# Kernel optimization log

Hardware: AMD Instinct MI355X
Metric: run time of the kernel (lower is better)

Reference implementation:

```python
import jax, jax.numpy as jnp
import numpy as np
import math

B, M, DM = 8, 512, 1024
H, DH = 16, 64
DFF = 4096
RA, RF, RO = 32, 384, 384
EPS = 1e-12  # BERT LayerNorm eps


def layernorm(x, g, b):
    mu = jnp.mean(x, axis=-1, keepdims=True)
    var = jnp.mean(jnp.square(x - mu), axis=-1, keepdims=True)
    return (x - mu) * jax.lax.rsqrt(var + EPS) * g + b


def setup_inputs() -> dict:
    key = jax.random.key(0)
    ks = jax.random.split(key, 24)
    s = 0.02
    inp = {
        "x": jax.random.normal(ks[0], (B, M, DM), jnp.float32),
        "mask": jnp.zeros((B, M), jnp.float32),  # additive attention mask
        "Pq": jax.random.normal(ks[1], (H, DM, RA), jnp.float32) * s,
        "Vq": jax.random.normal(ks[2], (H, RA, DH), jnp.float32) * s,
        "Pk": jax.random.normal(ks[3], (H, DM, RA), jnp.float32) * s,
        "Vk": jax.random.normal(ks[4], (H, RA, DH), jnp.float32) * s,
        "Pv": jax.random.normal(ks[5], (H, DM, RA), jnp.float32) * s,
        "Vv": jax.random.normal(ks[6], (H, RA, DH), jnp.float32) * s,
        "bq": jax.random.normal(ks[7], (H, DH), jnp.float32) * s,
        "bk": jax.random.normal(ks[8], (H, DH), jnp.float32) * s,
        "bv": jax.random.normal(ks[9], (H, DH), jnp.float32) * s,
        "Uo": jax.random.normal(ks[10], (DM, RO), jnp.float32) * s,
        "Vo": jax.random.normal(ks[11], (RO, DM), jnp.float32) * s,
        "bo_attn": jax.random.normal(ks[12], (DM,), jnp.float32) * s,
        "U1": jax.random.normal(ks[13], (DM, RF), jnp.float32) * s,
        "V1": jax.random.normal(ks[14], (RF, DFF), jnp.float32) * s,
        "b1": jax.random.normal(ks[15], (DFF,), jnp.float32) * s,
        "U2": jax.random.normal(ks[16], (DFF, RF), jnp.float32) * s,
        "V2": jax.random.normal(ks[17], (RF, DM), jnp.float32) * s,
        "b2": jax.random.normal(ks[18], (DM,), jnp.float32) * s,
        "ln1_g": jnp.ones((DM,), jnp.float32),
        "ln1_b": jnp.zeros((DM,), jnp.float32),
        "ln2_g": jnp.ones((DM,), jnp.float32),
        "ln2_b": jnp.zeros((DM,), jnp.float32),
    }
    return inp


def reference(x, mask, Pq, Vq, Pk, Vk, Pv, Vv, bq, bk, bv,
              Uo, Vo, bo_attn, U1, V1, b1, U2, V2, b2,
              ln1_g, ln1_b, ln2_g, ln2_b):
    b_, m_, dm = x.shape
    h = Pq.shape[0]
    dh = dm // h
    # low-rank per-head projections: x -> [B,H,M,R] -> [B,H,M,dh]
    q = jnp.einsum('bmd,hdr->bhmr', x, Pq)
    k = jnp.einsum('bmd,hdr->bhmr', x, Pk)
    v = jnp.einsum('bmd,hdr->bhmr', x, Pv)
    Q = jnp.einsum('bhmr,hrd->bhmd', q, Vq) + bq[None, :, None, :]
    K = jnp.einsum('bhmr,hrd->bhmd', k, Vk) + bk[None, :, None, :]
    V = jnp.einsum('bhmr,hrd->bhmd', v, Vv) + bv[None, :, None, :]
    # scaled dot-product attention (flash_svd_attention equivalent)
    scores = jnp.einsum('bhmd,bhnd->bhmn', Q, K) / math.sqrt(dh)
    scores = scores + mask[:, None, None, :]
    probs = jax.nn.softmax(scores, axis=-1)
    attn = jnp.einsum('bhmn,bhnd->bhmd', probs, V)  # [B,H,M,dh]
    attn = attn.transpose(0, 2, 1, 3).reshape(b_, m_, dm)
    # low-rank output projection + residual + LN
    x1 = layernorm(x + (attn @ Uo) @ Vo + bo_attn, ln1_g, ln1_b)
    # flashsvd_ffn_v1 equivalent: gelu((x1 @ U1) @ V1 + b1) @ U2 @ V2 + b2
    mid = x1 @ U1
    hdn = jax.nn.gelu(mid @ V1 + b1, approximate=False)
    y = (hdn @ U2) @ V2 + b2
    out = layernorm(x1 + y, ln2_g, ln2_b)
    return out
```

## Files before the change

### kernel.cpp

```cpp
#include <hip/hip_runtime.h>
#include <math.h>

typedef __attribute__((ext_vector_type(8))) short short8;
typedef __attribute__((ext_vector_type(4))) float floatx4;

__device__ inline unsigned short f2bf(float f){
    union { float f; unsigned u; } v; v.f = f;
    unsigned r = v.u + 0x7fffu + ((v.u >> 16) & 1u);
    return (unsigned short)(r >> 16);
}
__device__ inline float bf2f(unsigned short b){
    union { unsigned u; float f; } v; v.u = ((unsigned)b) << 16;
    return v.f;
}
__device__ inline unsigned short to_bf(float f){ return f2bf(f); }
__device__ inline unsigned short to_bf(unsigned short u){ return u; }

#define GLD_LDS16(g, l) __builtin_amdgcn_global_load_lds( \
    (const __attribute__((address_space(1))) void*)(g),   \
    (__attribute__((address_space(3))) void*)(l), 16, 0, 0)

__global__ __launch_bounds__(256) void cast_kernel(const float* __restrict__ s,
                                                   unsigned short* __restrict__ d){
    int i = (blockIdx.x*256 + threadIdx.x)*4;
    float4 v = *(const float4*)(s+i);
    ushort4 o; o.x=f2bf(v.x); o.y=f2bf(v.y); o.z=f2bf(v.z); o.w=f2bf(v.w);
    *(ushort4*)(d+i) = o;
}

__global__ __launch_bounds__(256) void castP_kernel(
    const float* __restrict__ p0, const float* __restrict__ p1,
    const float* __restrict__ p2, unsigned short* __restrict__ d){
    int blk = blockIdx.x;
    int proj = blk >> 9;
    const float* s = (proj==0)?p0:(proj==1)?p1:p2;
    int off = (blk & 511)*1024 + threadIdx.x*4;
    float4 v = *(const float4*)(s+off);
    ushort4 o; o.x=f2bf(v.x); o.y=f2bf(v.y); o.z=f2bf(v.z); o.w=f2bf(v.w);
    *(ushort4*)(d + (size_t)proj*524288 + off) = o;
}

__global__ __launch_bounds__(256) void reduce4_kernel(
    const float* __restrict__ p, unsigned short* __restrict__ o, long mn){
    long i = ((long)blockIdx.x*256 + threadIdx.x)*4;
    float4 a = *(const float4*)(p+i);
    float4 b = *(const float4*)(p+mn+i);
    float4 c = *(const float4*)(p+2*mn+i);
    float4 d = *(const float4*)(p+3*mn+i);
    ushort4 r;
    r.x = f2bf(a.x+b.x+c.x+d.x); r.y = f2bf(a.y+b.y+c.y+d.y);
    r.z = f2bf(a.z+b.z+c.z+d.z); r.w = f2bf(a.w+b.w+c.w+d.w);
    *(ushort4*)(o+i) = r;
}

__global__ __launch_bounds__(256) void bcat_kernel(
    const float* __restrict__ bq, const float* __restrict__ bk,
    const float* __restrict__ bv, float* __restrict__ bcat){
    int i = blockIdx.x*256 + threadIdx.x;
    const float* p = (i < 1024) ? bq : (i < 2048) ? bk : bv;
    bcat[i] = p[i & 1023];
}

template<typename T>
__global__ __launch_bounds__(256) void trans_kernel(
    const T* __restrict__ src, unsigned short* __restrict__ dst,
    int R, int C, long sz, long dz)
{
    __shared__ unsigned short tile[32][33];
    const T* s = src + (size_t)blockIdx.z * sz;
    unsigned short* d = dst + (size_t)blockIdx.z * dz;
    int c0 = blockIdx.x*32, r0 = blockIdx.y*32;
    int tr = threadIdx.x>>3, tc = (threadIdx.x&7)*4;
    const T* sp = s + (size_t)(r0+tr)*C + c0 + tc;
#pragma unroll
    for (int i=0;i<4;i++) tile[tr][tc+i] = to_bf(sp[i]);
    __syncthreads();
    ushort4 o; o.x = tile[tc+0][tr]; o.y = tile[tc+1][tr];
    o.z = tile[tc+2][tr]; o.w = tile[tc+3][tr];
    *(ushort4*)(d + (size_t)(c0+tr)*R + r0 + tc) = o;
}

__global__ __launch_bounds__(256) void trans2_kernel(
    const float* __restrict__ s0, unsigned short* __restrict__ d0,
    const float* __restrict__ s1, unsigned short* __restrict__ d1,
    int R, int C)
{
    __shared__ unsigned short tile[32][33];
    const float* s = blockIdx.z ? s1 : s0;
    unsigned short* d = blockIdx.z ? d1 : d0;
    int c0 = blockIdx.x*32, r0 = blockIdx.y*32;
    int tr = threadIdx.x>>3, tc = (threadIdx.x&7)*4;
    const float* sp = s + (size_t)(r0+tr)*C + c0 + tc;
#pragma unroll
    for (int i=0;i<4;i++) tile[tr][tc+i] = f2bf(sp[i]);
    __syncthreads();
    ushort4 o; o.x = tile[tc+0][tr]; o.y = tile[tc+1][tr];
    o.z = tile[tc+2][tr]; o.w = tile[tc+3][tr];
    *(ushort4*)(d + (size_t)(c0+tr)*R + r0 + tc) = o;
}

__global__ __launch_bounds__(256) void vtrans3_kernel(
    const float* __restrict__ v0, const float* __restrict__ v1,
    const float* __restrict__ v2, unsigned short* __restrict__ dst)
{
    __shared__ unsigned short tile[32][33];
    int z = blockIdx.z;
    int proj = z >> 4, h = z & 15;
    const float* s = ((proj==0)?v0:(proj==1)?v1:v2) + h*2048;
    unsigned short* d = dst + (size_t)proj*32768 + h*2048;
    int c0 = blockIdx.x*32;
    int tr = threadIdx.x>>3, tc = (threadIdx.x&7)*4;
    const float* sp = s + (size_t)tr*64 + c0 + tc;
#pragma unroll
    for (int i=0;i<4;i++) tile[tr][tc+i] = f2bf(sp[i]);
    __syncthreads();
    ushort4 o; o.x = tile[tc+0][tr]; o.y = tile[tc+1][tr];
    o.z = tile[tc+2][tr]; o.w = tile[tc+3][tr];
    *(ushort4*)(d + (size_t)(c0+tr)*32 + tc) = o;
}

__global__ __launch_bounds__(256) void mm64_kernel(
    const unsigned short* __restrict__ A, const unsigned short* __restrict__ Bt,
    unsigned short* __restrict__ C, int Kdim, int lda, int ldb, int ldc,
    long ah, long al, long bh, long bl, long ch, long cl)
{
    __shared__ unsigned short As[64*40];
    __shared__ unsigned short Bs[64*40];
    int z = blockIdx.z;
    const unsigned short* Ab = A + (size_t)(z>>4)*ah + (size_t)(z&15)*al;
    const unsigned short* Bb = Bt + (size_t)(z>>4)*bh + (size_t)(z&15)*bl;
    int row0 = blockIdx.y*64, col0 = blockIdx.x*64;
    int t = threadIdx.x;
    int ar = t>>2, ak = (t&3)*8;
    int w = t>>6, lane = t&63, quad = lane>>4, c16 = lane&15;
    int wm = (w&1)*32, wn = (w>>1)*32;

    floatx4 zero = {0.f,0.f,0.f,0.f};
    floatx4 acc[2][2];
    acc[0][0]=zero; acc[0][1]=zero; acc[1][0]=zero; acc[1][1]=zero;

    const unsigned short* Ap = Ab + (size_t)(row0+ar)*lda + ak;
    const unsigned short* Bp = Bb + (size_t)(col0+ar)*ldb + ak;

    for (int kk=0; kk<Kdim; kk+=32){
        uint4 av = *(const uint4*)(Ap + kk);
        uint4 bv = *(const uint4*)(Bp + kk);
        __syncthreads();
        *(uint4*)(As + ar*40 + ak) = av;
        *(uint4*)(Bs + ar*40 + ak) = bv;
        __syncthreads();
        short8 a0 = *(const short8*)(As + (wm   +c16)*40 + quad*8);
        short8 a1 = *(const short8*)(As + (wm+16+c16)*40 + quad*8);
        short8 b0 = *(const short8*)(Bs + (wn   +c16)*40 + quad*8);
        short8 b1 = *(const short8*)(Bs + (wn+16+c16)*40 + quad*8);
        acc[0][0] = __builtin_amdgcn_mfma_f32_16x16x32_bf16(a0,b0,acc[0][0],0,0,0);
        acc[0][1] = __builtin_amdgcn_mfma_f32_16x16x32_bf16(a0,b1,acc[0][1],0,0,0);
        acc[1][0] = __builtin_amdgcn_mfma_f32_16x16x32_bf16(a1,b0,acc[1][0],0,0,0);
        acc[1][1] = __builtin_amdgcn_mfma_f32_16x16x32_bf16(a1,b1,acc[1][1],0,0,0);
    }

    size_t zc = (size_t)(z>>4)*ch + (size_t)(z&15)*cl;
#pragma unroll
    for (int mt=0; mt<2; mt++)
#pragma unroll
    for (int r=0; r<4; r++){
        int row = row0 + wm + mt*16 + quad*4 + r;
#pragma unroll
        for (int nt=0; nt<2; nt++){
            int col = col0 + wn + nt*16 + c16;
            C[zc + (size_t)row*ldc + col] = f2bf(acc[mt][nt][r]);
        }
    }
}

template<int EPI>
__global__ __launch_bounds__(256) void mm128_kernel(
    const unsigned short* __restrict__ A, const unsigned short* __restrict__ Bt,
    void* __restrict__ C, int Kdim, int lda, int ldb, int ldc,
    const float* __restrict__ aux, const float* __restrict__ resid)
{
    __shared__ unsigned short As[128*64];
    __shared__ unsigned short Bs[128*64];
    int row0 = blockIdx.y*128, col0 = blockIdx.x*128;
    int t = threadIdx.x;
    int w = t>>6, lane = t&63, quad = lane>>4, c16 = lane&15;
    int wm = (w&1)*64, wn = (w>>1)*64;

    int srow = lane>>3;
    int kc = (lane&7) ^ srow;
    const unsigned short* Ag = A + (size_t)(row0 + w*32 + srow)*lda + kc*8;
    const unsigned short* Bg = Bt + (size_t)(col0 + w*32 + srow)*ldb + kc*8;
    unsigned short* AsW = As + (w*32)*64;
    unsigned short* BsW = Bs + (w*32)*64;

    floatx4 acc[4][4];
#pragma unroll
    for (int i=0;i<4;i++)
#pragma unroll
    for (int j=0;j<4;j++) acc[i][j] = (floatx4){0.f,0.f,0.f,0.f};

    int xa = (c16&7)*8;

    for (int kk=0; kk<Kdim; kk+=64){
#pragma unroll
        for (int i=0;i<4;i++){
            GLD_LDS16(Ag + (size_t)(i*8)*lda + kk, AsW + i*512);
            GLD_LDS16(Bg + (size_t)(i*8)*ldb + kk, BsW + i*512);
        }
        __syncthreads();
#pragma unroll
        for (int ks=0; ks<2; ks++){
            short8 a[4], b[4];
#pragma unroll
            for (int mt=0; mt<4; mt++)
                a[mt] = *(const short8*)(As + (wm + mt*16 + c16)*64
                                            + (((ks*4 + quad)*8) ^ xa));
#pragma unroll
            for (int nt=0; nt<4; nt++)
                b[nt] = *(const short8*)(Bs + (wn + nt*16 + c16)*64
                                            + (((ks*4 + quad)*8) ^ xa));
#pragma unroll
            for (int mt=0; mt<4; mt++)
#pragma unroll
                for (int nt=0; nt<4; nt++)
                    acc[mt][nt] = __builtin_amdgcn_mfma_f32_16x16x32_bf16(
                        a[mt], b[nt], acc[mt][nt], 0,0,0);
        }
        __syncthreads();
    }

#pragma unroll
    for (int mt=0; mt<4; mt++)
#pragma unroll
    for (int r=0; r<4; r++){
        int row = row0 + wm + mt*16 + quad*4 + r;
#pragma unroll
        for (int nt=0; nt<4; nt++){
            int col = col0 + wn + nt*16 + c16;
            float v = acc[mt][nt][r];
            if (EPI==0) {
                ((unsigned short*)C)[(size_t)row*ldc + col] = f2bf(v);
            } else if (EPI==2) {
                v += aux[col];
                v = 0.5f*v*(1.0f + erff(v*0.70710678118654752f));
                ((unsigned short*)C)[(size_t)row*ldc + col] = f2bf(v);
            } else if (EPI==3) {
                ((float*)C)[(size_t)row*ldc + col] =
                    v + aux[col] + resid[(size_t)row*ldc + col];
            } else {
                int proj = col >> 10, cw = col & 1023;
                int b_ = row >> 9, m_ = row & 511;
                size_t idx = (size_t)proj*4194304
                           + ((size_t)(b_*16 + (cw>>6))*512 + m_)*64 + (cw&63);
                ((unsigned short*)C)[idx] = f2bf(v + aux[col]);
            }
        }
    }
}

__global__ __launch_bounds__(256) void mmsk_kernel(
    const unsigned short* __restrict__ A, const unsigned short* __restrict__ Bt,
    float* __restrict__ Cp, int Kchunk, int lda, int ldb, int ldc, long mn)
{
    __shared__ unsigned short As[128*64];
    __shared__ unsigned short Bs[128*64];
    int row0 = blockIdx.y*128, col0 = blockIdx.x*128;
    int t = threadIdx.x;
    int w = t>>6, lane = t&63, quad = lane>>4, c16 = lane&15;
    int wm = (w&1)*64, wn = (w>>1)*64;

    int srow = lane>>3;
    int kc = (lane&7) ^ srow;
    const unsigned short* Ag = A + (size_t)(row0 + w*32 + srow)*lda + kc*8;
    const unsigned short* Bg = Bt + (size_t)(col0 + w*32 + srow)*ldb + kc*8;
    unsigned short* AsW = As + (w*32)*64;
    unsigned short* BsW = Bs + (w*32)*64;

    floatx4 acc[4][4];
#pragma unroll
    for (int i=0;i<4;i++)
#pragma unroll
    for (int j=0;j<4;j++) acc[i][j] = (floatx4){0.f,0.f,0.f,0.f};

    int xa = (c16&7)*8;
    int k0 = blockIdx.z * Kchunk;
    for (int kk=k0; kk<k0+Kchunk; kk+=64){
#pragma unroll
        for (int i=0;i<4;i++){
            GLD_LDS16(Ag + (size_t)(i*8)*lda + kk, AsW + i*512);
            GLD_LDS16(Bg + (size_t)(i*8)*ldb + kk, BsW + i*512);
        }
        __syncthreads();
#pragma unroll
        for (int ks=0; ks<2; ks++){
            short8 a[4], b[4];
#pragma unroll
            for (int mt=0; mt<4; mt++)
                a[mt] = *(const short8*)(As + (wm + mt*16 + c16)*64
                                            + (((ks*4 + quad)*8) ^ xa));
#pragma unroll
            for (int nt=0; nt<4; nt++)
                b[nt] = *(const short8*)(Bs + (wn + nt*16 + c16)*64
                                            + (((ks*4 + quad)*8) ^ xa));
#pragma unroll
            for (int mt=0; mt<4; mt++)
#pragma unroll
                for (int nt=0; nt<4; nt++)
                    acc[mt][nt] = __builtin_amdgcn_mfma_f32_16x16x32_bf16(
                        a[mt], b[nt], acc[mt][nt], 0,0,0);
        }
        __syncthreads();
    }

    float* Cz = Cp + (size_t)blockIdx.z * mn;
#pragma unroll
    for (int mt=0; mt<4; mt++)
#pragma unroll
    for (int r=0; r<4; r++){
        int row = row0 + wm + mt*16 + quad*4 + r;
#pragma unroll
        for (int nt=0; nt<4; nt++){
            int col = col0 + wn + nt*16 + c16;
            Cz[(size_t)row*ldc + col] = acc[mt][nt][r];
        }
    }
}

__global__ __launch_bounds__(256) void flash_kernel(
    const unsigned short* __restrict__ Qb, const unsigned short* __restrict__ Kb,
    const unsigned short* __restrict__ Vt, const float* __restrict__ mask,
    unsigned short* __restrict__ attn)
{
    __shared__ unsigned short Qs[128*64];
    __shared__ unsigned short Ks[64*64];
    __shared__ unsigned short Vts[64*64];
    __shared__ unsigned short Ps[4][32*68];

    int qt = blockIdx.x, bh = blockIdx.y;
    int b = bh >> 4, h = bh & 15;
    int t = threadIdx.x;
    int w = t>>6, lane = t&63, quad = lane>>4, c16 = lane&15;

    const unsigned short* Qtile = Qb + ((size_t)bh*512 + qt*128)*64;
    const unsigned short* Ktile0 = Kb + (size_t)bh*512*64;
    const unsigned short* Vtbh = Vt + (size_t)bh*32768;

#pragma unroll
    for (int i=0;i<4;i++){
        GLD_LDS16(Qtile + (size_t)(w*32 + i*8)*64 + lane*8, Qs + (w*32+i*8)*64);
    }

    floatx4 Oacc[2][4];
#pragma unroll
    for (int mt=0;mt<2;mt++)
#pragma unroll
    for (int nd=0;nd<4;nd++) Oacc[mt][nd] = (floatx4){0.f,0.f,0.f,0.f};
    float mrow[2][4], lrow[2][4];
#pragma unroll
    for (int mt=0;mt<2;mt++)
#pragma unroll
    for (int r=0;r<4;r++){ mrow[mt][r] = -3.0e38f; lrow[mt][r] = 0.f; }

    unsigned short* Pw = &Ps[w][0];

    for (int kt=0; kt<8; kt++){
        __syncthreads();
#pragma unroll
        for (int i=0;i<2;i++){
            GLD_LDS16(Ktile0 + (size_t)(kt*64 + w*16 + i*8)*64 + lane*8,
                      Ks + (w*16+i*8)*64);
            GLD_LDS16(Vtbh + (size_t)(w*16 + i*8 + (lane>>3))*512 + kt*64 + (lane&7)*8,
                      Vts + (w*16+i*8)*64);
        }
        __syncthreads();

        floatx4 Sacc[2][4];
#pragma unroll
        for (int mt=0;mt<2;mt++)
#pragma unroll
        for (int nt=0;nt<4;nt++) Sacc[mt][nt] = (floatx4){0.f,0.f,0.f,0.f};
#pragma unroll
        for (int ks=0; ks<2; ks++){
            short8 a[2], bfr[4];
#pragma unroll
            for (int mt=0;mt<2;mt++)
                a[mt] = *(const short8*)(Qs + (w*32 + mt*16 + c16)*64 + ks*32 + quad*8);
#pragma unroll
            for (int nt=0;nt<4;nt++)
                bfr[nt] = *(const short8*)(Ks + (nt*16 + c16)*64 + ks*32 + quad*8);
#pragma unroll
            for (int mt=0;mt<2;mt++)
#pragma unroll
            for (int nt=0;nt<4;nt++)
                Sacc[mt][nt] = __builtin_amdgcn_mfma_f32_16x16x32_bf16(
                    a[mt], bfr[nt], Sacc[mt][nt], 0,0,0);
        }

        float mv[4];
#pragma unroll
        for (int nt=0;nt<4;nt++)
            mv[nt] = mask[b*512 + kt*64 + nt*16 + c16];

#pragma unroll
        for (int mt=0;mt<2;mt++)
#pragma unroll
        for (int r=0;r<4;r++){
            float sv[4];
#pragma unroll
            for (int nt=0;nt<4;nt++) sv[nt] = Sacc[mt][nt][r]*0.125f + mv[nt];
            float rmax = fmaxf(fmaxf(sv[0],sv[1]), fmaxf(sv[2],sv[3]));
            rmax = fmaxf(rmax, __shfl_xor(rmax, 1));
            rmax = fmaxf(rmax, __shfl_xor(rmax, 2));
            rmax = fmaxf(rmax, __shfl_xor(rmax, 4));
            rmax = fmaxf(rmax, __shfl_xor(rmax, 8));
            float mold = mrow[mt][r];
            float mnew = fmaxf(mold, rmax);
            float alpha = __expf(mold - mnew);
            float p[4], ps = 0.f;
#pragma unroll
            for (int nt=0;nt<4;nt++){ p[nt] = __expf(sv[nt]-mnew); ps += p[nt]; }
            ps += __shfl_xor(ps, 1);
            ps += __shfl_xor(ps, 2);
            ps += __shfl_xor(ps, 4);
            ps += __shfl_xor(ps, 8);
            lrow[mt][r] = lrow[mt][r]*alpha + ps;
            mrow[mt][r] = mnew;
#pragma unroll
            for (int nd=0;nd<4;nd++) Oacc[mt][nd][r] *= alpha;
#pragma unroll
            for (int nt=0;nt<4;nt++)
                Pw[(mt*16 + quad*4 + r)*68 + nt*16 + c16] = f2bf(p[nt]);
        }

#pragma unroll
        for (int ks=0; ks<2; ks++){
            short8 a[2], bfr[4];
#pragma unroll
            for (int mt=0;mt<2;mt++)
                a[mt] = *(const short8*)(Pw + (mt*16 + c16)*68 + ks*32 + quad*8);
#pragma unroll
            for (int nd=0;nd<4;nd++)
                bfr[nd] = *(const short8*)(Vts + (nd*16 + c16)*64 + ks*32 + quad*8);
#pragma unroll
            for (int mt=0;mt<2;mt++)
#pragma unroll
            for (int nd=0;nd<4;nd++)
                Oacc[mt][nd] = __builtin_amdgcn_mfma_f32_16x16x32_bf16(
                    a[mt], bfr[nd], Oacc[mt][nd], 0,0,0);
        }
    }

#pragma unroll
    for (int mt=0;mt<2;mt++)
#pragma unroll
    for (int r=0;r<4;r++){
        int m = qt*128 + w*32 + mt*16 + quad*4 + r;
        float inv = 1.0f / lrow[mt][r];
        unsigned short* op = attn + ((size_t)(b*512 + m))*1024 + h*64;
#pragma unroll
        for (int nd=0;nd<4;nd++)
            op[nd*16 + c16] = f2bf(Oacc[mt][nd][r] * inv);
    }
}

template<int DUAL>
__global__ __launch_bounds__(256) void ln_kernel(
    const float* __restrict__ in, const float* __restrict__ g,
    const float* __restrict__ bta, float* __restrict__ outf,
    unsigned short* __restrict__ outb)
{
    int row = blockIdx.x;
    int t = threadIdx.x;
    const float* x = in + (size_t)row*1024;
    float4 xv = ((const float4*)x)[t];
    float s  = xv.x + xv.y + xv.z + xv.w;
    float ss = xv.x*xv.x + xv.y*xv.y + xv.z*xv.z + xv.w*xv.w;
#pragma unroll
    for (int off=32; off>0; off>>=1){ s += __shfl_down(s, off); ss += __shfl_down(ss, off); }
    __shared__ float rs[4], rss[4];
    int wid = t>>6, lane = t&63;
    if (lane==0){ rs[wid]=s; rss[wid]=ss; }
    __syncthreads();
    s  = rs[0]+rs[1]+rs[2]+rs[3];
    ss = rss[0]+rss[1]+rss[2]+rss[3];
    float mu  = s * (1.0f/1024.0f);
    float var = ss * (1.0f/1024.0f) - mu*mu;
    float inv = rsqrtf(var + 1e-12f);
    float4 gv = ((const float4*)g)[t];
    float4 bv = ((const float4*)bta)[t];
    float4 o = make_float4((xv.x-mu)*inv*gv.x+bv.x, (xv.y-mu)*inv*gv.y+bv.y,
                           (xv.z-mu)*inv*gv.z+bv.z, (xv.w-mu)*inv*gv.w+bv.w);
    ((float4*)(outf + (size_t)row*1024))[t] = o;
    if (DUAL){
        ushort4 ob; ob.x=f2bf(o.x); ob.y=f2bf(o.y); ob.z=f2bf(o.z); ob.w=f2bf(o.w);
        ((ushort4*)(outb + (size_t)row*1024))[t] = ob;
    }
}

extern "C" void kernel_launch(void* const* d_in, const int* in_sizes, int n_in,
                              void* d_out, int out_size, void* d_ws, size_t ws_size,
                              hipStream_t stream)
{
    const float* x       = (const float*)d_in[0];
    const float* mask    = (const float*)d_in[1];
    const float* Pq      = (const float*)d_in[2];
    const float* Vq      = (const float*)d_in[3];
    const float* Pk      = (const float*)d_in[4];
    const float* Vk      = (const float*)d_in[5];
    const float* Pv      = (const float*)d_in[6];
    const float* Vv      = (const float*)d_in[7];
    const float* bq      = (const float*)d_in[8];
    const float* bk      = (const float*)d_in[9];
    const float* bv      = (const float*)d_in[10];
    const float* Uo      = (const float*)d_in[11];
    const float* Vo      = (const float*)d_in[12];
    const float* bo_attn = (const float*)d_in[13];
    const float* U1      = (const float*)d_in[14];
    const float* V1      = (const float*)d_in[15];
    const float* b1      = (const float*)d_in[16];
    const float* U2      = (const float*)d_in[17];
    const float* V2      = (const float*)d_in[18];
    const float* b2      = (const float*)d_in[19];
    const float* ln1_g   = (const float*)d_in[20];
    const float* ln1_b   = (const float*)d_in[21];
    const float* ln2_g   = (const float*)d_in[22];
    const float* ln2_b   = (const float*)d_in[23];
    float* out = (float*)d_out;

    char* base = (char*)d_ws;
    unsigned short* Uo_t   = (unsigned short*)(base + 0);
    unsigned short* Vo_t   = (unsigned short*)(base + 786432);
    unsigned short* U1_t   = (unsigned short*)(base + 1572864);
    unsigned short* V1_t   = (unsigned short*)(base + 2359296);
    unsigned short* U2_t   = (unsigned short*)(base + 5505024);
    unsigned short* V2_t   = (unsigned short*)(base + 8650752);
    float*          bcat   = (float*)(base + 9437184);
    unsigned short* Wt     = (unsigned short*)(base + 9449472);
    unsigned short* Pbf    = (unsigned short*)(base + 15740928);
    unsigned short* Vt2    = (unsigned short*)(base + 18886656);
    unsigned short* x_bf   = (unsigned short*)(base + 19083264);
    unsigned short* t_bf   = (unsigned short*)(base + 9449472);
    float*          ybuf   = (float*)(base + 12595200);
    float*          x1     = (float*)(base + 29372416);
    unsigned short* x1_bf  = (unsigned short*)(base + 46149632);
    unsigned short* hdn_bf = (unsigned short*)(base + 54538240);
    float*          part0  = (float*)(base + 12595200);
    float*          part1  = (float*)(base + 54538240);
    float*          part2  = (float*)(base + 88092672);
    unsigned short* Qb     = (unsigned short*)(base + 76558336);
    unsigned short* Kb     = (unsigned short*)(base + 84946944);
    unsigned short* Vb     = (unsigned short*)(base + 93535552);
    unsigned short* Vt     = (unsigned short*)(base + 101924160);
    unsigned short* attn_bf= (unsigned short*)(base + 110312768);

    const long MN384 = 4096L*384;

    cast_kernel<<<4096,256,0,stream>>>(x, x_bf);
    castP_kernel<<<1536,256,0,stream>>>(Pq, Pk, Pv, Pbf);
    vtrans3_kernel<<<dim3(2,1,48),256,0,stream>>>(Vq, Vk, Vv, Vt2);
    bcat_kernel<<<12,256,0,stream>>>(bq, bk, bv, bcat);
    trans2_kernel<<<dim3(12,32,2),256,0,stream>>>(Uo, Uo_t, U1, U1_t, 1024, 384);
    trans2_kernel<<<dim3(32,12,2),256,0,stream>>>(Vo, Vo_t, V2, V2_t, 384, 1024);
    trans_kernel<float><<<dim3(128,12,1),256,0,stream>>>(V1, V1_t, 384,4096, 0,0);
    trans_kernel<float><<<dim3(12,128,1),256,0,stream>>>(U2, U2_t, 4096,384, 0,0);

    mm64_kernel<<<dim3(16,1,48),256,0,stream>>>(Vt2, Pbf, Wt,
        32, 32, 32, 1024, 32768,2048, 524288,32768, 1048576,65536);

    mm128_kernel<4><<<dim3(24,32,1),256,0,stream>>>(x_bf, Wt, Qb,
        1024, 1024, 1024, 3072, bcat, nullptr);

    trans_kernel<unsigned short><<<dim3(2,16,128),256,0,stream>>>(Vb, Vt, 512,64, 32768,32768);

    flash_kernel<<<dim3(4,128),256,0,stream>>>(Qb, Kb, Vt, mask, attn_bf);

    mmsk_kernel<<<dim3(3,32,4),256,0,stream>>>(attn_bf, Uo_t, part0,
        256, 1024, 1024, 384, MN384);
    reduce4_kernel<<<1536,256,0,stream>>>(part0, t_bf, MN384);
    mm128_kernel<3><<<dim3(8,32,1),256,0,stream>>>(t_bf, Vo_t, ybuf,
        384, 384, 384, 1024, bo_attn, x);
    ln_kernel<1><<<4096,256,0,stream>>>(ybuf, ln1_g, ln1_b, x1, x1_bf);
    mmsk_kernel<<<dim3(3,32,4),256,0,stream>>>(x1_bf, U1_t, part1,
        256, 1024, 1024, 384, MN384);
    reduce4_kernel<<<1536,256,0,stream>>>(part1, t_bf, MN384);
    mm128_kernel<2><<<dim3(32,32,1),256,0,stream>>>(t_bf, V1_t, hdn_bf,
        384, 384, 384, 4096, b1, nullptr);
    mmsk_kernel<<<dim3(3,32,4),256,0,stream>>>(hdn_bf, U2_t, part2,
        1024, 4096, 4096, 384, MN384);
    reduce4_kernel<<<1536,256,0,stream>>>(part2, t_bf, MN384);
    mm128_kernel<3><<<dim3(8,32,1),256,0,stream>>>(t_bf, V2_t, ybuf,
        384, 384, 384, 1024, b2, x1);
    ln_kernel<0><<<4096,256,0,stream>>>(ybuf, ln2_g, ln2_b, out, nullptr);
}
```

Measured before the change: 378.6 us.

## Fuse V transpose and Q scaling into QKV epilogue; restructure flash attention tiles

The QKV GEMM epilogue now writes V directly in transposed layout and pre-scales Q by 1/sqrt(dh), which removes the separate V transpose kernel and the per-score scale multiply. The flash kernel now processes 64 query rows per block with 16 rows per wave, so the grid doubles. Q fragments are held in registers instead of LDS, the mask is folded into the accumulator init, and K/V/P LDS tiles use an XOR swizzle to avoid bank conflicts. The epilogue's V stores become strided scatter writes, and K/V tiles are reloaded twice as often across blocks.

Result: no change. 375.2 us (-0.9%).

```diff
diff --git a/kernel.cpp b/kernel.cpp
--- a/kernel.cpp
+++ b/kernel.cpp
@@ -250,9 +250,15 @@
             } else {
                 int proj = col >> 10, cw = col & 1023;
                 int b_ = row >> 9, m_ = row & 511;
-                size_t idx = (size_t)proj*4194304
-                           + ((size_t)(b_*16 + (cw>>6))*512 + m_)*64 + (cw&63);
-                ((unsigned short*)C)[idx] = f2bf(v + aux[col]);
+                int hh = cw >> 6, dd = cw & 63;
+                float vv = v + aux[col];
+                if (proj == 0) vv *= 0.125f;
+                size_t idx;
+                if (proj == 2)
+                    idx = (size_t)2*4194304 + ((size_t)(b_*16+hh)*64 + dd)*512 + m_;
+                else
+                    idx = (size_t)proj*4194304 + ((size_t)(b_*16+hh)*512 + m_)*64 + dd;
+                ((unsigned short*)C)[idx] = f2bf(vv);
             }
         }
     }
@@ -331,35 +337,33 @@
     const unsigned short* __restrict__ Vt, const float* __restrict__ mask,
     unsigned short* __restrict__ attn)
 {
-    __shared__ unsigned short Qs[128*64];
     __shared__ unsigned short Ks[64*64];
     __shared__ unsigned short Vts[64*64];
-    __shared__ unsigned short Ps[4][32*68];
+    __shared__ unsigned short Ps[4][16*64];
 
     int qt = blockIdx.x, bh = blockIdx.y;
     int b = bh >> 4, h = bh & 15;
     int t = threadIdx.x;
     int w = t>>6, lane = t&63, quad = lane>>4, c16 = lane&15;
 
-    const unsigned short* Qtile = Qb + ((size_t)bh*512 + qt*128)*64;
+    int qrow = qt*64 + w*16 + c16;
+    const unsigned short* Qp = Qb + ((size_t)bh*512 + qrow)*64 + quad*8;
+    short8 qf0 = *(const short8*)(Qp);
+    short8 qf1 = *(const short8*)(Qp + 32);
+
     const unsigned short* Ktile0 = Kb + (size_t)bh*512*64;
     const unsigned short* Vtbh = Vt + (size_t)bh*32768;
 
-#pragma unroll
-    for (int i=0;i<4;i++){
-        GLD_LDS16(Qtile + (size_t)(w*32 + i*8)*64 + lane*8, Qs + (w*32+i*8)*64);
-    }
-
-    floatx4 Oacc[2][4];
-#pragma unroll
-    for (int mt=0;mt<2;mt++)
-#pragma unroll
-    for (int nd=0;nd<4;nd++) Oacc[mt][nd] = (floatx4){0.f,0.f,0.f,0.f};
-    float mrow[2][4], lrow[2][4];
-#pragma unroll
-    for (int mt=0;mt<2;mt++)
-#pragma unroll
-    for (int r=0;r<4;r++){ mrow[mt][r] = -3.0e38f; lrow[mt][r] = 0.f; }
+    int srow = lane>>3;
+    int kc = (lane&7) ^ srow;
+    int xa = (c16&7)*8;
+
+    floatx4 Oacc[4];
+#pragma unroll
+    for (int nd=0;nd<4;nd++) Oacc[nd] = (floatx4){0.f,0.f,0.f,0.f};
+    float mrow[4], lrow[4];
+#pragma unroll
+    for (int r=0;r<4;r++){ mrow[r] = -3.0e38f; lrow[r] = 0.f; }
 
     unsigned short* Pw = &Ps[w][0];
 
@@ -367,99 +371,88 @@
         __syncthreads();
 #pragma unroll
         for (int i=0;i<2;i++){
-            GLD_LDS16(Ktile0 + (size_t)(kt*64 + w*16 + i*8)*64 + lane*8,
+            GLD_LDS16(Ktile0 + (size_t)(kt*64 + w*16 + i*8 + srow)*64 + kc*8,
                       Ks + (w*16+i*8)*64);
-            GLD_LDS16(Vtbh + (size_t)(w*16 + i*8 + (lane>>3))*512 + kt*64 + (lane&7)*8,
+            GLD_LDS16(Vtbh + (size_t)(w*16 + i*8 + srow)*512 + kt*64 + kc*8,
                       Vts + (w*16+i*8)*64);
         }
         __syncthreads();
 
-        floatx4 Sacc[2][4];
-#pragma unroll
-        for (int mt=0;mt<2;mt++)
-#pragma unroll
-        for (int nt=0;nt<4;nt++) Sacc[mt][nt] = (floatx4){0.f,0.f,0.f,0.f};
+        floatx4 Sacc[4];
+#pragma unroll
+        for (int nt=0;nt<4;nt++){
+            float mv = mask[b*512 + kt*64 + nt*16 + c16];
+            Sacc[nt] = (floatx4){mv,mv,mv,mv};
+        }
 #pragma unroll
         for (int ks=0; ks<2; ks++){
-            short8 a[2], bfr[4];
-#pragma unroll
-            for (int mt=0;mt<2;mt++)
-                a[mt] = *(const short8*)(Qs + (w*32 + mt*16 + c16)*64 + ks*32 + quad*8);
+            short8 qk = ks ? qf1 : qf0;
+            short8 bfr[4];
 #pragma unroll
             for (int nt=0;nt<4;nt++)
-                bfr[nt] = *(const short8*)(Ks + (nt*16 + c16)*64 + ks*32 + quad*8);
-#pragma unroll
-            for (int mt=0;mt<2;mt++)
+                bfr[nt] = *(const short8*)(Ks + (nt*16 + c16)*64
+                                              + (((ks*4 + quad)*8) ^ xa));
 #pragma unroll
             for (int nt=0;nt<4;nt++)
-                Sacc[mt][nt] = __builtin_amdgcn_mfma_f32_16x16x32_bf16(
-                    a[mt], bfr[nt], Sacc[mt][nt], 0,0,0);
-        }
-
-        float mv[4];
-#pragma unroll
-        for (int nt=0;nt<4;nt++)
-            mv[nt] = mask[b*512 + kt*64 + nt*16 + c16];
-
-#pragma unroll
-        for (int mt=0;mt<2;mt++)
+                Sacc[nt] = __builtin_amdgcn_mfma_f32_16x16x32_bf16(
+                    qk, bfr[nt], Sacc[nt], 0,0,0);
+        }
+
 #pragma unroll
         for (int r=0;r<4;r++){
-            float sv[4];
-#pragma unroll
-            for (int nt=0;nt<4;nt++) sv[nt] = Sacc[mt][nt][r]*0.125f + mv[nt];
-            float rmax = fmaxf(fmaxf(sv[0],sv[1]), fmaxf(sv[2],sv[3]));
+            float sv0 = Sacc[0][r], sv1 = Sacc[1][r],
+                  sv2 = Sacc[2][r], sv3 = Sacc[3][r];
+            float rmax = fmaxf(fmaxf(sv0,sv1), fmaxf(sv2,sv3));
             rmax = fmaxf(rmax, __shfl_xor(rmax, 1));
             rmax = fmaxf(rmax, __shfl_xor(rmax, 2));
             rmax = fmaxf(rmax, __shfl_xor(rmax, 4));
             rmax = fmaxf(rmax, __shfl_xor(rmax, 8));
-            float mold = mrow[mt][r];
+            float mold = mrow[r];
             float mnew = fmaxf(mold, rmax);
             float alpha = __expf(mold - mnew);
-            float p[4], ps = 0.f;
-#pragma unroll
-            for (int nt=0;nt<4;nt++){ p[nt] = __expf(sv[nt]-mnew); ps += p[nt]; }
+            float p0 = __expf(sv0-mnew), p1 = __expf(sv1-mnew);
+            float p2 = __expf(sv2-mnew), p3 = __expf(sv3-mnew);
+            float ps = p0+p1+p2+p3;
             ps += __shfl_xor(ps, 1);
             ps += __shfl_xor(ps, 2);
             ps += __shfl_xor(ps, 4);
             ps += __shfl_xor(ps, 8);
-            lrow[mt][r] = lrow[mt][r]*alpha + ps;
-            mrow[mt][r] = mnew;
-#pragma unroll
-            for (int nd=0;nd<4;nd++) Oacc[mt][nd][r] *= alpha;
-#pragma unroll
-            for (int nt=0;nt<4;nt++)
-                Pw[(mt*16 + quad*4 + r)*68 + nt*16 + c16] = f2bf(p[nt]);
+            lrow[r] = lrow[r]*alpha + ps;
+            mrow[r] = mnew;
+#pragma unroll
+            for (int nd=0;nd<4;nd++) Oacc[nd][r] *= alpha;
+            int rl = quad*4 + r;
+            int rx = rl & 7;
+            int cb = rl*64 + (c16&7);
+            Pw[cb + (((0*2 + (c16>>3)) ^ rx)*8)] = f2bf(p0);
+            Pw[cb + (((1*2 + (c16>>3)) ^ rx)*8)] = f2bf(p1);
+            Pw[cb + (((2*2 + (c16>>3)) ^ rx)*8)] = f2bf(p2);
+            Pw[cb + (((3*2 + (c16>>3)) ^ rx)*8)] = f2bf(p3);
         }
 
 #pragma unroll
         for (int ks=0; ks<2; ks++){
-            short8 a[2], bfr[4];
-#pragma unroll
-            for (int mt=0;mt<2;mt++)
-                a[mt] = *(const short8*)(Pw + (mt*16 + c16)*68 + ks*32 + quad*8);
+            short8 pa = *(const short8*)(Pw + c16*64 + (((ks*4 + quad)*8) ^ xa));
+            short8 bfr[4];
 #pragma unroll
             for (int nd=0;nd<4;nd++)
-                bfr[nd] = *(const short8*)(Vts + (nd*16 + c16)*64 + ks*32 + quad*8);
-#pragma unroll
-            for (int mt=0;mt<2;mt++)
+                bfr[nd] = *(const short8*)(Vts + (nd*16 + c16)*64
+                                               + (((ks*4 + quad)*8) ^ xa));
 #pragma unroll
             for (int nd=0;nd<4;nd++)
-                Oacc[mt][nd] = __builtin_amdgcn_mfma_f32_16x16x32_bf16(
-                    a[mt], bfr[nd], Oacc[mt][nd], 0,0,0);
-        }
-    }
-
-#pragma unroll
-    for (int mt=0;mt<2;mt++)
+                Oacc[nd] = __builtin_amdgcn_mfma_f32_16x16x32_bf16(
+                    pa, bfr[nd], Oacc[nd], 0,0,0);
+        }
+    }
+
 #pragma unroll
     for (int r=0;r<4;r++){
-        int m = qt*128 + w*32 + mt*16 + quad*4 + r;
-        float inv = 1.0f / lrow[mt][r];
+        int m = qt*64 + w*16 + quad*4 + r;
+        float inv = 1.0f / lrow[r];
         unsigned short* op = attn + ((size_t)(b*512 + m))*1024 + h*64;
 #pragma unroll
         for (int nd=0;nd<4;nd++)
-            op[nd*16 + c16] = f2bf(Oacc[mt][nd][r] * inv);
+            op[nd*16 + c16] = f2bf(Oacc[nd][r] * inv);
     }
 }
 
@@ -549,8 +542,7 @@
     float*          part2  = (float*)(base + 88092672);
     unsigned short* Qb     = (unsigned short*)(base + 76558336);
     unsigned short* Kb     = (unsigned short*)(base + 84946944);
-    unsigned short* Vb     = (unsigned short*)(base + 93535552);
-    unsigned short* Vt     = (unsigned short*)(base + 101924160);
+    unsigned short* Vt     = (unsigned short*)(base + 93535552);
     unsigned short* attn_bf= (unsigned short*)(base + 110312768);
 
     const long MN384 = 4096L*384;
@@ -570,9 +562,7 @@
     mm128_kernel<4><<<dim3(24,32,1),256,0,stream>>>(x_bf, Wt, Qb,
         1024, 1024, 1024, 3072, bcat, nullptr);
 
-    trans_kernel<unsigned short><<<dim3(2,16,128),256,0,stream>>>(Vb, Vt, 512,64, 32768,32768);
-
-    flash_kernel<<<dim3(4,128),256,0,stream>>>(Qb, Kb, Vt, mask, attn_bf);
+    flash_kernel<<<dim3(8,128),256,0,stream>>>(Qb, Kb, Vt, mask, attn_bf);
 
     mmsk_kernel<<<dim3(3,32,4),256,0,stream>>>(attn_bf, Uo_t, part0,
         256, 1024, 1024, 384, MN384);
```
